# Optimization experiments

Measured on AMD Instinct MI355X. Metric: run time of the kernel, lower is better.

## Reference

```python
import jax, jax.numpy as jnp
import numpy as np

N_HEAD = 12
D_HEAD = 64  # key_dim // n_head = 768 // 12


def sparsemax(z):
    # Martins & Astudillo (2016): projection of each row of z onto the simplex.
    K = z.shape[-1]
    z_sorted = -jnp.sort(-z, axis=-1)                      # descending sort
    cs = jnp.cumsum(z_sorted, axis=-1)
    r = jnp.arange(1, K + 1, dtype=z.dtype)
    support = (1.0 + r * z_sorted) > cs                    # support set indicator
    ksz = jnp.sum(support, axis=-1, keepdims=True)         # support size k(z)
    cs_k = jnp.take_along_axis(cs, ksz.astype(jnp.int32) - 1, axis=-1)
    tau = (cs_k - 1.0) / ksz.astype(z.dtype)               # threshold
    return jnp.maximum(z - tau, 0.0)


def setup_inputs() -> dict:
    key = jax.random.key(0)
    kq, kk, kv, kwq, kbq, kwk, kbk = jax.random.split(key, 7)
    B, L, D = 8, 1024, 768
    scale = 0.02
    return {
        "q": jax.random.normal(kq, (B, L, D), jnp.float32),
        "k": jax.random.normal(kk, (B, L, D), jnp.float32),
        "v": jax.random.normal(kv, (B, L, D), jnp.float32),
        "Wq": jax.random.normal(kwq, (D, D), jnp.float32) * scale,  # torch Linear weight [out,in]
        "bq": jax.random.normal(kbq, (D,), jnp.float32) * scale,
        "Wk": jax.random.normal(kwk, (D, D), jnp.float32) * scale,
        "bk": jax.random.normal(kbk, (D,), jnp.float32) * scale,
    }


def reference(q, k, v, Wq, bq, Wk, bk):
    B, Lq, _ = q.shape
    Lkv = k.shape[1]
    # project and split heads: [B, H, L, d_head]
    qh = (q @ Wq.T + bq).reshape(B, Lq, N_HEAD, D_HEAD).transpose(0, 2, 1, 3)
    kh = (k @ Wk.T + bk).reshape(B, Lkv, N_HEAD, D_HEAD).transpose(0, 2, 1, 3)
    inv_sqrt_d = jnp.asarray(1.0 / np.sqrt(D_HEAD), q.dtype)
    scores = jnp.einsum("bhqd,bhkd->bhqk", qh, kh) * inv_sqrt_d  # [B,H,Lq,Lkv]
    attn = sparsemax(scores)
    attn = attn.mean(axis=1)                                      # head-mean -> [B,Lq,Lkv]
    # eval mode: smooth_max is identity (training-only smoothing)
    output = jnp.einsum("bqk,bkd->bqd", attn, v)                  # [B,Lq,Dv]
    return output, attn
```

## Files before the change

kernel.cpp:

```cpp
#include <hip/hip_runtime.h>

#define BSZ 8
#define NH 12
#define LSEQ 1024
#define DMODEL 768
#define DHEAD 64
#define OUT_ELEMS 6291456
#define ATTN_ELEMS 8388608

typedef __attribute__((ext_vector_type(8))) short short8;
typedef __attribute__((ext_vector_type(4))) float f32x4;

__device__ __forceinline__ int   f2i(float x) { union { float f; int i; } c; c.f = x; return c.i; }
__device__ __forceinline__ float i2f(int x)   { union { int i; float f; } c; c.i = x; return c.f; }

__device__ __forceinline__ unsigned short f2bf(float x) {
    union { float f; unsigned u; } c; c.f = x;
    unsigned r = (c.u + 0x7FFF + ((c.u >> 16) & 1)) >> 16;
    return (unsigned short)r;
}
__device__ __forceinline__ float bf2f(unsigned short h) {
    union { float f; unsigned u; } c; c.u = ((unsigned)h) << 16;
    return c.f;
}
__device__ __forceinline__ void split2(float x, unsigned short& h, unsigned short& l) {
    h = f2bf(x);
    l = f2bf(x - bf2f(h));
}

template<int CTRL>
__device__ __forceinline__ float dppadd(float v) {
    return v + i2f(__builtin_amdgcn_update_dpp(0, f2i(v), CTRL, 0xF, 0xF, true));
}
template<int CTRL>
__device__ __forceinline__ float dppmax(float v) {
    return fmaxf(v, i2f(__builtin_amdgcn_update_dpp(f2i(v), f2i(v), CTRL, 0xF, 0xF, false)));
}

__device__ __forceinline__ void wsum2(float s[2]) {
#define WS(CTRL) _Pragma("unroll") for (int rr = 0; rr < 2; ++rr) { s[rr] = dppadd<CTRL>(s[rr]); }
    WS(0x111) WS(0x112) WS(0x114) WS(0x118) WS(0x142) WS(0x143)
#undef WS
#pragma unroll
    for (int rr = 0; rr < 2; ++rr) s[rr] = i2f(__builtin_amdgcn_readlane(f2i(s[rr]), 63));
}

__device__ __forceinline__ void wred3(float& s, float& q, float& m) {
#define WS(CTRL) { s = dppadd<CTRL>(s); q = dppadd<CTRL>(q); m = dppmax<CTRL>(m); }
    WS(0x111) WS(0x112) WS(0x114) WS(0x118) WS(0x142) WS(0x143)
#undef WS
    s = i2f(__builtin_amdgcn_readlane(f2i(s), 63));
    q = i2f(__builtin_amdgcn_readlane(f2i(q), 63));
    m = i2f(__builtin_amdgcn_readlane(f2i(m), 63));
}

__global__ __launch_bounds__(256) void proj_mfma(
    const float* __restrict__ qin, const float* __restrict__ kin,
    const float* __restrict__ Wq, const float* __restrict__ bq,
    const float* __restrict__ Wk, const float* __restrict__ bk,
    unsigned short* __restrict__ ws) {
    const float* A; const float* W; const float* bias;
    unsigned short* hi; unsigned short* lo;
    if (blockIdx.z == 0) { A = qin; W = Wq; bias = bq; hi = ws;                lo = ws + OUT_ELEMS; }
    else                 { A = kin; W = Wk; bias = bk; hi = ws + 2*OUT_ELEMS; lo = ws + 3*OUT_ELEMS; }

    __shared__ unsigned short Ah[128][32], Al[128][32];
    __shared__ unsigned short Bh[128][32], Bl[128][32];

    const int t    = threadIdx.x;
    const int lane = t & 63;
    const int w    = t >> 6;
    const int wr   = w >> 1, wc = w & 1;
    const int mrow = lane & 15, quad = lane >> 4;
    const int m0   = blockIdx.y * 128;
    const int n0   = blockIdx.x * 128;

    const int srow = t >> 3;
    const int scol = (t & 7) * 4;

    f32x4 acc[4][4];
#pragma unroll
    for (int i = 0; i < 4; ++i)
#pragma unroll
        for (int j = 0; j < 4; ++j) acc[i][j] = (f32x4){0.f, 0.f, 0.f, 0.f};

    for (int k0 = 0; k0 < DMODEL; k0 += 32) {
        float4 av[4], wv[4];
#pragma unroll
        for (int i = 0; i < 4; ++i) {
            av[i] = *(const float4*)&A[(size_t)(m0 + srow + i * 32) * DMODEL + k0 + scol];
            wv[i] = *(const float4*)&W[(size_t)(n0 + srow + i * 32) * DMODEL + k0 + scol];
        }
        __syncthreads();
#pragma unroll
        for (int i = 0; i < 4; ++i) {
            ushort4 h4, l4;
            split2(av[i].x, h4.x, l4.x); split2(av[i].y, h4.y, l4.y);
            split2(av[i].z, h4.z, l4.z); split2(av[i].w, h4.w, l4.w);
            *(ushort4*)&Ah[srow + i * 32][scol] = h4;
            *(ushort4*)&Al[srow + i * 32][scol] = l4;
            split2(wv[i].x, h4.x, l4.x); split2(wv[i].y, h4.y, l4.y);
            split2(wv[i].z, h4.z, l4.z); split2(wv[i].w, h4.w, l4.w);
            *(ushort4*)&Bh[srow + i * 32][scol] = h4;
            *(ushort4*)&Bl[srow + i * 32][scol] = l4;
        }
        __syncthreads();

        short8 ah[4], al[4], bh[4], bl[4];
#pragma unroll
        for (int i = 0; i < 4; ++i) {
            ah[i] = *(const short8*)&Ah[wr * 64 + i * 16 + mrow][quad * 8];
            al[i] = *(const short8*)&Al[wr * 64 + i * 16 + mrow][quad * 8];
            bh[i] = *(const short8*)&Bh[wc * 64 + i * 16 + mrow][quad * 8];
            bl[i] = *(const short8*)&Bl[wc * 64 + i * 16 + mrow][quad * 8];
        }
#pragma unroll
        for (int i = 0; i < 4; ++i)
#pragma unroll
            for (int j = 0; j < 4; ++j) {
                acc[i][j] = __builtin_amdgcn_mfma_f32_16x16x32_bf16(al[i], bh[j], acc[i][j], 0, 0, 0);
                acc[i][j] = __builtin_amdgcn_mfma_f32_16x16x32_bf16(ah[i], bl[j], acc[i][j], 0, 0, 0);
                acc[i][j] = __builtin_amdgcn_mfma_f32_16x16x32_bf16(ah[i], bh[j], acc[i][j], 0, 0, 0);
            }
    }

#pragma unroll
    for (int j = 0; j < 4; ++j) {
        const int ng = n0 + wc * 64 + j * 16 + mrow;
        const float bj = bias[ng];
        const int hh = ng >> 6, dd = ng & 63;
#pragma unroll
        for (int i = 0; i < 4; ++i) {
#pragma unroll
            for (int reg = 0; reg < 4; ++reg) {
                const int mg = m0 + wr * 64 + i * 16 + quad * 4 + reg;
                const float c = acc[i][j][reg] + bj;
                unsigned short ch, cl;
                split2(c, ch, cl);
                const size_t idx = (((size_t)(mg >> 10) * NH + hh) * LSEQ + (mg & 1023)) * DHEAD + dd;
                hi[idx] = ch;
                lo[idx] = cl;
            }
        }
    }
}

__global__ __launch_bounds__(1024, 8) void attn_kernel(
    const unsigned short* __restrict__ ws, float* __restrict__ attn_out) {
    __shared__ float S[16 * 1024];

    const unsigned short* Qhi = ws;
    const unsigned short* Qlo = ws + OUT_ELEMS;
    const unsigned short* Khi = ws + 2 * OUT_ELEMS;
    const unsigned short* Klo = ws + 3 * OUT_ELEMS;

    const int t = threadIdx.x;
    const int lane = t & 63;
    const int w = t >> 6;
    const int idlin = blockIdx.x;
    const int b  = idlin & 7;
    const int q0 = (idlin >> 3) * 16;

    const int mrow = lane & 15;
    const int quad = lane >> 4;

    float macc[16];
#pragma unroll
    for (int j = 0; j < 16; ++j) macc[j] = 0.f;

#pragma unroll 1
    for (int h = 0; h < NH; ++h) {
        const size_t hb = ((size_t)b * NH + h) * (LSEQ * DHEAD);

        {
            const size_t aoff = hb + (size_t)(q0 + mrow) * DHEAD + quad * 8;
            short8 qh0 = *(const short8*)(Qhi + aoff);
            short8 qh1 = *(const short8*)(Qhi + aoff + 32);
            short8 ql0 = *(const short8*)(Qlo + aoff);
            short8 ql1 = *(const short8*)(Qlo + aoff + 32);
#pragma unroll
            for (int nt = 0; nt < 4; ++nt) {
                const int n0 = w * 64 + nt * 16;
                const size_t boff = hb + (size_t)(n0 + mrow) * DHEAD + quad * 8;
                short8 kh0 = *(const short8*)(Khi + boff);
                short8 kh1 = *(const short8*)(Khi + boff + 32);
                short8 kl0 = *(const short8*)(Klo + boff);
                short8 kl1 = *(const short8*)(Klo + boff + 32);
                f32x4 d = (f32x4){0.f, 0.f, 0.f, 0.f};
                d = __builtin_amdgcn_mfma_f32_16x16x32_bf16(ql0, kh0, d, 0, 0, 0);
                d = __builtin_amdgcn_mfma_f32_16x16x32_bf16(qh0, kl0, d, 0, 0, 0);
                d = __builtin_amdgcn_mfma_f32_16x16x32_bf16(qh0, kh0, d, 0, 0, 0);
                d = __builtin_amdgcn_mfma_f32_16x16x32_bf16(ql1, kh1, d, 0, 0, 0);
                d = __builtin_amdgcn_mfma_f32_16x16x32_bf16(qh1, kl1, d, 0, 0, 0);
                d = __builtin_amdgcn_mfma_f32_16x16x32_bf16(qh1, kh1, d, 0, 0, 0);
                const int swcol = (n0 + mrow) ^ (quad << 4);
#pragma unroll
                for (int reg = 0; reg < 4; ++reg)
                    S[(quad * 4 + reg) * 1024 + swcol] = d[reg] * 0.125f;
            }
        }
        __syncthreads();

        float z[16];
        {
            const int swz = ((w >> 2) & 3) << 4;
#pragma unroll
            for (int c = 0; c < 4; ++c)
                *(f32x4*)&z[c * 4] = *(const f32x4*)&S[w * 1024 + ((c * 256 + lane * 4) ^ swz)];
        }
        __syncthreads();

        float sv, qv, mv;
        {
            float s0 = 0.f, s1 = 0.f, s2 = 0.f, s3 = 0.f;
            float p0 = 0.f, p1 = 0.f, p2 = 0.f, p3 = 0.f;
            float m0 = z[0], m1 = z[1], m2 = z[2], m3 = z[3];
#pragma unroll
            for (int j = 0; j < 16; j += 4) {
                s0 += z[j]; s1 += z[j + 1]; s2 += z[j + 2]; s3 += z[j + 3];
                p0 = fmaf(z[j],     z[j],     p0);
                p1 = fmaf(z[j + 1], z[j + 1], p1);
                p2 = fmaf(z[j + 2], z[j + 2], p2);
                p3 = fmaf(z[j + 3], z[j + 3], p3);
            }
#pragma unroll
            for (int j = 4; j < 16; j += 4) {
                m0 = fmaxf(m0, z[j]);     m1 = fmaxf(m1, z[j + 1]);
                m2 = fmaxf(m2, z[j + 2]); m3 = fmaxf(m3, z[j + 3]);
            }
            sv = (s0 + s1) + (s2 + s3);
            qv = (p0 + p1) + (p2 + p3);
            mv = fmaxf(fmaxf(m0, m1), fmaxf(m2, m3));
        }
        wred3(sv, qv, mv);

        const float t0s = fmaxf((sv - 1.0f) * (1.0f / 1024.0f), mv - 1.0f);
        float tau;
        {
            const float mu  = sv * (1.0f / 1024.0f);
            const float var = fmaxf(qv * (1.0f / 1024.0f) - mu * mu, 1e-12f);
            const float sg  = sqrtf(var);
            const float a   = 2.7196f + 0.33333f * __logf(sg);
            const float tg  = mu + (a - 0.25f) * sg;
            tau = fminf(fmaxf(tg, t0s), mv - 1e-3f);
        }

#define SP_PASS(SC) do { \
        float a0 = 0.f, a1 = 0.f, a2 = 0.f, a3 = 0.f; \
        float n0 = 0.f, n1 = 0.f, n2 = 0.f, n3 = 0.f; \
        _Pragma("unroll") for (int j = 0; j < 16; j += 4) { \
            bool g0 = z[j]     > tau; \
            bool g1 = z[j + 1] > tau; \
            bool g2 = z[j + 2] > tau; \
            bool g3 = z[j + 3] > tau; \
            a0 += g0 ? z[j]     : 0.f;  n0 += g0 ? 1.f : 0.f; \
            a1 += g1 ? z[j + 1] : 0.f;  n1 += g1 ? 1.f : 0.f; \
            a2 += g2 ? z[j + 2] : 0.f;  n2 += g2 ? 1.f : 0.f; \
            a3 += g3 ? z[j + 3] : 0.f;  n3 += g3 ? 1.f : 0.f; \
        } \
        SC[0] = (a0 + a1) + (a2 + a3); \
        SC[1] = (n0 + n1) + (n2 + n3); \
        wsum2(SC); \
} while (0)

        float prev;
        {
            float sc[2];
            SP_PASS(sc);
            const float tn = (sc[0] - 1.0f) / sc[1];
            if (tn >= tau) { tau = tn; prev = sc[1]; }
            else           { tau = t0s; prev = -1.f; }
        }
        for (int it = 0; it < 63; ++it) {
            float sc[2];
            SP_PASS(sc);
            if (sc[1] == prev) break;
            tau = (sc[0] - 1.0f) / sc[1];
            prev = sc[1];
        }
#undef SP_PASS

#pragma unroll
        for (int j = 0; j < 16; ++j)
            macc[j] += fmaxf(z[j] - tau, 0.f);
    }

    float* ao = attn_out + ((size_t)b * LSEQ + q0) * LSEQ;
#pragma unroll
    for (int c = 0; c < 4; ++c) {
        f32x4 o;
#pragma unroll
        for (int j = 0; j < 4; ++j) o[j] = macc[c * 4 + j] * (1.0f / 12.0f);
        *(f32x4*)&ao[(size_t)w * LSEQ + c * 256 + lane * 4] = o;
    }
}

__global__ __launch_bounds__(256) void out_mfma(
    const float* __restrict__ attn, const float* __restrict__ v,
    float* __restrict__ out) {
    const int b = blockIdx.z;
    const float* Ab = attn + (size_t)b * LSEQ * LSEQ;
    const float* Vb = v    + (size_t)b * LSEQ * DMODEL;
    float* Cb       = out  + (size_t)b * LSEQ * DMODEL;

    __shared__ unsigned short Ah[128][32], Al[128][32];
    __shared__ unsigned short Bh[128][36], Bl[128][36];

    const int t    = threadIdx.x;
    const int lane = t & 63;
    const int w    = t >> 6;
    const int wr   = w >> 1, wc = w & 1;
    const int mrow = lane & 15, quad = lane >> 4;
    const int m0   = blockIdx.y * 128;
    const int n0   = blockIdx.x * 128;

    const int srow = t >> 3;
    const int scol = (t & 7) * 4;
    const int bn   = t & 127;
    const int bk0  = (t >> 7) * 16;

    f32x4 acc[4][4];
#pragma unroll
    for (int i = 0; i < 4; ++i)
#pragma unroll
        for (int j = 0; j < 4; ++j) acc[i][j] = (f32x4){0.f, 0.f, 0.f, 0.f};

    for (int k0 = 0; k0 < LSEQ; k0 += 32) {
        float4 av[4];
#pragma unroll
        for (int i = 0; i < 4; ++i)
            av[i] = *(const float4*)&Ab[(size_t)(m0 + srow + i * 32) * LSEQ + k0 + scol];
        float bv[16];
#pragma unroll
        for (int i = 0; i < 16; ++i)
            bv[i] = Vb[(size_t)(k0 + bk0 + i) * DMODEL + n0 + bn];

        __syncthreads();
#pragma unroll
        for (int i = 0; i < 4; ++i) {
            ushort4 h4, l4;
            split2(av[i].x, h4.x, l4.x); split2(av[i].y, h4.y, l4.y);
            split2(av[i].z, h4.z, l4.z); split2(av[i].w, h4.w, l4.w);
            *(ushort4*)&Ah[srow + i * 32][scol] = h4;
            *(ushort4*)&Al[srow + i * 32][scol] = l4;
        }
#pragma unroll
        for (int g = 0; g < 4; ++g) {
            ushort4 h4, l4;
            split2(bv[g * 4 + 0], h4.x, l4.x); split2(bv[g * 4 + 1], h4.y, l4.y);
            split2(bv[g * 4 + 2], h4.z, l4.z); split2(bv[g * 4 + 3], h4.w, l4.w);
            *(ushort4*)&Bh[bn][bk0 + g * 4] = h4;
            *(ushort4*)&Bl[bn][bk0 + g * 4] = l4;
        }
        __syncthreads();

        short8 ah[4], al[4], bh[4], bl[4];
#pragma unroll
        for (int i = 0; i < 4; ++i) {
            ah[i] = *(const short8*)&Ah[wr * 64 + i * 16 + mrow][quad * 8];
            al[i] = *(const short8*)&Al[wr * 64 + i * 16 + mrow][quad * 8];
        }
#pragma unroll
        for (int j = 0; j < 4; ++j) {
            const unsigned short* ph = &Bh[wc * 64 + j * 16 + mrow][quad * 8];
            const unsigned short* pl = &Bl[wc * 64 + j * 16 + mrow][quad * 8];
            uint2 h0 = *(const uint2*)ph;
            uint2 h1 = *(const uint2*)(ph + 4);
            uint2 l0 = *(const uint2*)pl;
            uint2 l1 = *(const uint2*)(pl + 4);
            union { uint u[4]; short8 s; } ch, cl;
            ch.u[0] = h0.x; ch.u[1] = h0.y; ch.u[2] = h1.x; ch.u[3] = h1.y;
            cl.u[0] = l0.x; cl.u[1] = l0.y; cl.u[2] = l1.x; cl.u[3] = l1.y;
            bh[j] = ch.s; bl[j] = cl.s;
        }
#pragma unroll
        for (int i = 0; i < 4; ++i)
#pragma unroll
            for (int j = 0; j < 4; ++j) {
                acc[i][j] = __builtin_amdgcn_mfma_f32_16x16x32_bf16(al[i], bh[j], acc[i][j], 0, 0, 0);
                acc[i][j] = __builtin_amdgcn_mfma_f32_16x16x32_bf16(ah[i], bl[j], acc[i][j], 0, 0, 0);
                acc[i][j] = __builtin_amdgcn_mfma_f32_16x16x32_bf16(ah[i], bh[j], acc[i][j], 0, 0, 0);
            }
    }

#pragma unroll
    for (int i = 0; i < 4; ++i)
#pragma unroll
        for (int j = 0; j < 4; ++j)
#pragma unroll
            for (int reg = 0; reg < 4; ++reg) {
                const int mg = m0 + wr * 64 + i * 16 + quad * 4 + reg;
                const int ng = n0 + wc * 64 + j * 16 + mrow;
                Cb[(size_t)mg * DMODEL + ng] = acc[i][j][reg];
            }
}

extern "C" void kernel_launch(void* const* d_in, const int* in_sizes, int n_in,
                              void* d_out, int out_size, void* d_ws, size_t ws_size,
                              hipStream_t stream) {
    const float* q  = (const float*)d_in[0];
    const float* k  = (const float*)d_in[1];
    const float* v  = (const float*)d_in[2];
    const float* Wq = (const float*)d_in[3];
    const float* bq = (const float*)d_in[4];
    const float* Wk = (const float*)d_in[5];
    const float* bk = (const float*)d_in[6];

    float* out  = (float*)d_out;
    float* attn = out + OUT_ELEMS;
    unsigned short* ws = (unsigned short*)d_ws;

    hipLaunchKernelGGL(proj_mfma, dim3(6, 64, 2), dim3(256), 0, stream,
                       q, k, Wq, bq, Wk, bk, ws);
    hipLaunchKernelGGL(attn_kernel, dim3(512), dim3(1024), 0, stream,
                       ws, attn);
    hipLaunchKernelGGL(out_mfma, dim3(6, 8, 8), dim3(256), 0, stream,
                       attn, v, out);
}
```

Baseline: 518.3 us.

## Fuse attn@V into sparsemax kernel using sparse support gather

Removes the separate dense attn@V MFMA GEMM and computes the output inside the attention kernel. Each wave ballots the nonzero sparsemax entries per head and accumulates only those V rows with scalar FMAs, relying on sparsemax output being sparse. This drops the second pass over the attention matrix and a kernel launch. In exchange it adds data-dependent serial loops and scattered V reads per head, and lowers the occupancy hint in launch bounds from 8 to 6.

Measured after the change: 821.4 us. +58.5%, slower.

```diff
diff --git a/kernel.cpp b/kernel.cpp
--- a/kernel.cpp
+++ b/kernel.cpp
@@ -145,8 +145,9 @@
     }
 }
 
-__global__ __launch_bounds__(1024, 8) void attn_kernel(
-    const unsigned short* __restrict__ ws, float* __restrict__ attn_out) {
+__global__ __launch_bounds__(1024, 6) void attn_kernel(
+    const unsigned short* __restrict__ ws, const float* __restrict__ vmat,
+    float* __restrict__ attn_out, float* __restrict__ out) {
     __shared__ float S[16 * 1024];
 
     const unsigned short* Qhi = ws;
@@ -164,9 +165,14 @@
     const int mrow = lane & 15;
     const int quad = lane >> 4;
 
+    const float* Vb = vmat + (size_t)b * LSEQ * DMODEL;
+
     float macc[16];
 #pragma unroll
     for (int j = 0; j < 16; ++j) macc[j] = 0.f;
+    float oacc[12];
+#pragma unroll
+    for (int d = 0; d < 12; ++d) oacc[d] = 0.f;
 
 #pragma unroll 1
     for (int h = 0; h < NH; ++h) {
@@ -281,8 +287,23 @@
 #undef SP_PASS
 
 #pragma unroll
-        for (int j = 0; j < 16; ++j)
-            macc[j] += fmaxf(z[j] - tau, 0.f);
+        for (int c = 0; c < 4; ++c) {
+#pragma unroll
+            for (int j = 0; j < 4; ++j) {
+                const float p = fmaxf(z[c * 4 + j] - tau, 0.f);
+                macc[c * 4 + j] += p;
+                unsigned long long msk = __ballot(p > 0.f);
+                while (msk) {
+                    const int s = __ffsll((unsigned long long)msk) - 1;
+                    msk &= msk - 1;
+                    const float pv = i2f(__builtin_amdgcn_readlane(f2i(p), s));
+                    const float* vr = Vb + (size_t)(c * 256 + s * 4 + j) * DMODEL;
+#pragma unroll
+                    for (int d = 0; d < 12; ++d)
+                        oacc[d] = fmaf(pv, vr[d * 64 + lane], oacc[d]);
+                }
+            }
+        }
     }
 
     float* ao = attn_out + ((size_t)b * LSEQ + q0) * LSEQ;
@@ -293,106 +314,10 @@
         for (int j = 0; j < 4; ++j) o[j] = macc[c * 4 + j] * (1.0f / 12.0f);
         *(f32x4*)&ao[(size_t)w * LSEQ + c * 256 + lane * 4] = o;
     }
-}
-
-__global__ __launch_bounds__(256) void out_mfma(
-    const float* __restrict__ attn, const float* __restrict__ v,
-    float* __restrict__ out) {
-    const int b = blockIdx.z;
-    const float* Ab = attn + (size_t)b * LSEQ * LSEQ;
-    const float* Vb = v    + (size_t)b * LSEQ * DMODEL;
-    float* Cb       = out  + (size_t)b * LSEQ * DMODEL;
-
-    __shared__ unsigned short Ah[128][32], Al[128][32];
-    __shared__ unsigned short Bh[128][36], Bl[128][36];
-
-    const int t    = threadIdx.x;
-    const int lane = t & 63;
-    const int w    = t >> 6;
-    const int wr   = w >> 1, wc = w & 1;
-    const int mrow = lane & 15, quad = lane >> 4;
-    const int m0   = blockIdx.y * 128;
-    const int n0   = blockIdx.x * 128;
-
-    const int srow = t >> 3;
-    const int scol = (t & 7) * 4;
-    const int bn   = t & 127;
-    const int bk0  = (t >> 7) * 16;
-
-    f32x4 acc[4][4];
-#pragma unroll
-    for (int i = 0; i < 4; ++i)
-#pragma unroll
-        for (int j = 0; j < 4; ++j) acc[i][j] = (f32x4){0.f, 0.f, 0.f, 0.f};
-
-    for (int k0 = 0; k0 < LSEQ; k0 += 32) {
-        float4 av[4];
-#pragma unroll
-        for (int i = 0; i < 4; ++i)
-            av[i] = *(const float4*)&Ab[(size_t)(m0 + srow + i * 32) * LSEQ + k0 + scol];
-        float bv[16];
-#pragma unroll
-        for (int i = 0; i < 16; ++i)
-            bv[i] = Vb[(size_t)(k0 + bk0 + i) * DMODEL + n0 + bn];
-
-        __syncthreads();
-#pragma unroll
-        for (int i = 0; i < 4; ++i) {
-            ushort4 h4, l4;
-            split2(av[i].x, h4.x, l4.x); split2(av[i].y, h4.y, l4.y);
-            split2(av[i].z, h4.z, l4.z); split2(av[i].w, h4.w, l4.w);
-            *(ushort4*)&Ah[srow + i * 32][scol] = h4;
-            *(ushort4*)&Al[srow + i * 32][scol] = l4;
-        }
-#pragma unroll
-        for (int g = 0; g < 4; ++g) {
-            ushort4 h4, l4;
-            split2(bv[g * 4 + 0], h4.x, l4.x); split2(bv[g * 4 + 1], h4.y, l4.y);
-            split2(bv[g * 4 + 2], h4.z, l4.z); split2(bv[g * 4 + 3], h4.w, l4.w);
-            *(ushort4*)&Bh[bn][bk0 + g * 4] = h4;
-            *(ushort4*)&Bl[bn][bk0 + g * 4] = l4;
-        }
-        __syncthreads();
-
-        short8 ah[4], al[4], bh[4], bl[4];
-#pragma unroll
-        for (int i = 0; i < 4; ++i) {
-            ah[i] = *(const short8*)&Ah[wr * 64 + i * 16 + mrow][quad * 8];
-            al[i] = *(const short8*)&Al[wr * 64 + i * 16 + mrow][quad * 8];
-        }
-#pragma unroll
-        for (int j = 0; j < 4; ++j) {
-            const unsigned short* ph = &Bh[wc * 64 + j * 16 + mrow][quad * 8];
-            const unsigned short* pl = &Bl[wc * 64 + j * 16 + mrow][quad * 8];
-            uint2 h0 = *(const uint2*)ph;
-            uint2 h1 = *(const uint2*)(ph + 4);
-            uint2 l0 = *(const uint2*)pl;
-            uint2 l1 = *(const uint2*)(pl + 4);
-            union { uint u[4]; short8 s; } ch, cl;
-            ch.u[0] = h0.x; ch.u[1] = h0.y; ch.u[2] = h1.x; ch.u[3] = h1.y;
-            cl.u[0] = l0.x; cl.u[1] = l0.y; cl.u[2] = l1.x; cl.u[3] = l1.y;
-            bh[j] = ch.s; bl[j] = cl.s;
-        }
-#pragma unroll
-        for (int i = 0; i < 4; ++i)
-#pragma unroll
-            for (int j = 0; j < 4; ++j) {
-                acc[i][j] = __builtin_amdgcn_mfma_f32_16x16x32_bf16(al[i], bh[j], acc[i][j], 0, 0, 0);
-                acc[i][j] = __builtin_amdgcn_mfma_f32_16x16x32_bf16(ah[i], bl[j], acc[i][j], 0, 0, 0);
-                acc[i][j] = __builtin_amdgcn_mfma_f32_16x16x32_bf16(ah[i], bh[j], acc[i][j], 0, 0, 0);
-            }
-    }
-
-#pragma unroll
-    for (int i = 0; i < 4; ++i)
-#pragma unroll
-        for (int j = 0; j < 4; ++j)
-#pragma unroll
-            for (int reg = 0; reg < 4; ++reg) {
-                const int mg = m0 + wr * 64 + i * 16 + quad * 4 + reg;
-                const int ng = n0 + wc * 64 + j * 16 + mrow;
-                Cb[(size_t)mg * DMODEL + ng] = acc[i][j][reg];
-            }
+    float* oo = out + ((size_t)b * LSEQ + q0 + w) * DMODEL;
+#pragma unroll
+    for (int d = 0; d < 12; ++d)
+        oo[d * 64 + lane] = oacc[d] * (1.0f / 12.0f);
 }
 
 extern "C" void kernel_launch(void* const* d_in, const int* in_sizes, int n_in,
@@ -413,7 +338,5 @@
     hipLaunchKernelGGL(proj_mfma, dim3(6, 64, 2), dim3(256), 0, stream,
                        q, k, Wq, bq, Wk, bk, ws);
     hipLaunchKernelGGL(attn_kernel, dim3(512), dim3(1024), 0, stream,
-                       ws, attn);
-    hipLaunchKernelGGL(out_mfma, dim3(6, 8, 8), dim3(256), 0, stream,
-                       attn, v, out);
-}
+                       ws, v, attn, out);
+}
```
